# Optimization experiments

Hardware: AMD Instinct MI355X
Metric: run time of the kernel (lower is better)

The kernel has to match this reference:

```python
import jax, jax.numpy as jnp
import numpy as np

N_NODES = 100000
N_GRAPHS = 512
NEG_SLOPE = 0.2


def gat_layer(x, src, dst, W, a_src, a_dst, b):
    # PyG GATConv (heads=1, concat=True, add_self_loops handled by caller via src/dst)
    h = x @ W                                   # [N, F]
    e = jax.nn.leaky_relu((h @ a_src)[src] + (h @ a_dst)[dst], NEG_SLOPE)  # [E]
    m = jax.ops.segment_max(e, dst, num_segments=N_NODES)
    ex = jnp.exp(e - m[dst])
    s = jax.ops.segment_sum(ex, dst, num_segments=N_NODES)
    alpha = ex / (s[dst] + 1e-16)               # per-destination softmax
    out = jax.ops.segment_sum(alpha[:, None] * h[src], dst, num_segments=N_NODES)
    return out + b


def setup_inputs() -> dict:
    key = jax.random.key(0)
    ks = jax.random.split(key, 12)
    x = jax.random.normal(ks[0], (N_NODES, 5), dtype=jnp.float32)
    edge_index = jax.random.randint(ks[1], (2, 3200000), 0, N_NODES, dtype=jnp.int64)
    batch = jnp.sort(jax.random.randint(ks[2], (N_NODES,), 0, N_GRAPHS, dtype=jnp.int64))
    def glorot(k, shape):
        lim = float(np.sqrt(6.0 / (shape[0] + shape[-1])))
        return jax.random.uniform(k, shape, jnp.float32, -lim, lim)
    return {
        "x": x, "edge_index": edge_index, "batch": batch,
        "W1": glorot(ks[3], (5, 16)), "as1": glorot(ks[4], (16,)), "ad1": glorot(ks[5], (16,)), "b1": jnp.zeros((16,), jnp.float32),
        "W2": glorot(ks[6], (16, 16)), "as2": glorot(ks[7], (16,)), "ad2": glorot(ks[8], (16,)), "b2": jnp.zeros((16,), jnp.float32),
        "Wf": glorot(ks[9], (16, 2)), "bf": jnp.zeros((2,), jnp.float32),
    }


def reference(x, edge_index, batch, W1, as1, ad1, b1, W2, as2, ad2, b2, Wf, bf):
    # add self-loops (PyG GATConv default)
    loop = jnp.arange(N_NODES, dtype=edge_index.dtype)
    src = jnp.concatenate([edge_index[0], loop])
    dst = jnp.concatenate([edge_index[1], loop])
    h = jax.nn.relu(gat_layer(x, src, dst, W1, as1, ad1, b1))
    h = jax.nn.relu(gat_layer(h, src, dst, W2, as2, ad2, b2))
    # global mean pool over graphs
    sums = jax.ops.segment_sum(h, batch, num_segments=N_GRAPHS)
    cnt = jax.ops.segment_sum(jnp.ones((N_NODES,), h.dtype), batch, num_segments=N_GRAPHS)
    pooled = sums / jnp.maximum(cnt, 1.0)[:, None]   # [G, 16]
    return pooled @ Wf + bf                          # [G, 2]
```

## Files before the change

kernel.cpp:

```cpp
#include <hip/hip_runtime.h>
#include <hip/hip_fp16.h>
#include <math.h>

#define N_NODES 100000
#define N_GRAPHS 512
#define F 16
#define NEG_SLOPE 0.2f
#define DMAX 80
#define NSLOT 64
#define NBUCK 391
#define BCAP 8704
#define EPB 16

__device__ __forceinline__ float lrelu(float v) {
    return v > 0.0f ? v : NEG_SLOPE * v;
}

__device__ __forceinline__ unsigned fkey(float f) {
    unsigned b = __float_as_uint(f);
    return (b & 0x80000000u) ? ~b : (b | 0x80000000u);
}
__device__ __forceinline__ float funkey(unsigned k) {
    unsigned b = (k & 0x80000000u) ? (k ^ 0x80000000u) : ~k;
    return __uint_as_float(b);
}

__global__ void k_part_prep(const int* __restrict__ esrc,
                            const int* __restrict__ edst, int E0, int nT,
                            int* __restrict__ bcur,
                            unsigned* __restrict__ bucket,
                            const float* __restrict__ x,
                            const float* __restrict__ W1,
                            const float* __restrict__ as1,
                            const float* __restrict__ ad1,
                            __half* __restrict__ h1,
                            float* __restrict__ ssrc,
                            float* __restrict__ sdst,
                            unsigned* __restrict__ cs1,
                            unsigned* __restrict__ cd1) {
    __shared__ int hist[NBUCK];
    __shared__ int gbase[NBUCK];
    __shared__ int off[NBUCK];
    __shared__ unsigned ls[4], ld[4];

    if ((int)blockIdx.x < nT) {
        int tbase = blockIdx.x * (blockDim.x * EPB);
        for (int i = threadIdx.x; i < NBUCK; i += blockDim.x) hist[i] = 0;
        __syncthreads();

        int rb[EPB];
        unsigned rv[EPB];
#pragma unroll
        for (int i = 0; i < EPB; ++i) {
            int e = tbase + i * blockDim.x + threadIdx.x;
            rb[i] = -1;
            if (e < E0) {
                int d = edst[e];
                int s = esrc[e];
                int b = d >> 8;
                rb[i] = b;
                rv[i] = (unsigned)s | ((unsigned)(d & 255) << 17);
                atomicAdd(&hist[b], 1);
            }
        }
        __syncthreads();

        for (int b = threadIdx.x; b < NBUCK; b += blockDim.x) {
            int h = hist[b];
            gbase[b] = h ? atomicAdd(&bcur[b], h) : 0;
            off[b] = 0;
        }
        __syncthreads();

#pragma unroll
        for (int i = 0; i < EPB; ++i) {
            int b = rb[i];
            if (b >= 0) {
                int p = gbase[b] + atomicAdd(&off[b], 1);
                if (p < BCAP) bucket[(size_t)b * BCAP + p] = rv[i];
            }
        }
    } else {
        int n = (blockIdx.x - nT) * blockDim.x + threadIdx.x;
        float ss = -INFINITY, sd = -INFINITY;
        if (n < N_NODES) {
            float xi[5];
#pragma unroll
            for (int i = 0; i < 5; ++i) xi[i] = x[n * 5 + i];
            ss = 0.f; sd = 0.f;
#pragma unroll
            for (int f = 0; f < F; ++f) {
                float acc = 0.f;
#pragma unroll
                for (int i = 0; i < 5; ++i) acc += xi[i] * W1[i * F + f];
                h1[n * F + f] = __float2half(acc);
                ss += acc * as1[f];
                sd += acc * ad1[f];
            }
            ssrc[n] = ss;
            sdst[n] = sd;
        }
        unsigned ks = fkey(ss), kd = fkey(sd);
#pragma unroll
        for (int o = 32; o; o >>= 1) {
            ks = max(ks, (unsigned)__shfl_xor((int)ks, o, 64));
            kd = max(kd, (unsigned)__shfl_xor((int)kd, o, 64));
        }
        int wid = threadIdx.x >> 6, lane = threadIdx.x & 63;
        if (lane == 0) { ls[wid] = ks; ld[wid] = kd; }
        __syncthreads();
        if (threadIdx.x == 0) {
            unsigned ms = ls[0], md = ld[0];
#pragma unroll
            for (int w = 1; w < 4; ++w) { ms = max(ms, ls[w]); md = max(md, ld[w]); }
            atomicMax(&cs1[blockIdx.x & (NSLOT - 1)], ms);
            atomicMax(&cd1[blockIdx.x & (NSLOT - 1)], md);
        }
    }
}

__global__ void k_fill2(const int* __restrict__ bcur,
                        const unsigned* __restrict__ bucket,
                        int* __restrict__ col,
                        int* __restrict__ deg) {
    int b = blockIdx.x;
    __shared__ int cur[256];
    if (threadIdx.x < 256) cur[threadIdx.x] = 0;
    __syncthreads();
    int cnt = min(bcur[b], BCAP);
    const unsigned* bk = bucket + (size_t)b * BCAP;
    for (int i = threadIdx.x; i < cnt; i += blockDim.x) {
        unsigned v = __builtin_nontemporal_load(&bk[i]);
        int s = (int)(v & 0x1FFFFu);
        int dl = (int)(v >> 17);
        int r = atomicAdd(&cur[dl], 1);
        if (r < DMAX) col[((size_t)((b << 8) | dl)) * DMAX + r] = s;
    }
    __syncthreads();
    if (threadIdx.x < 256) {
        int dst = (b << 8) | threadIdx.x;
        if (dst < N_NODES) deg[dst] = min(cur[threadIdx.x], DMAX);
    }
}

__device__ __forceinline__ float gat_aggregate(int n, int lane,
                                               const int* __restrict__ deg,
                                               const int* __restrict__ col,
                                               const float* __restrict__ ssrc,
                                               const float* __restrict__ sdst,
                                               const __half* __restrict__ h,
                                               const float* __restrict__ b,
                                               float c) {
    int dg = deg[n];
    size_t st = (size_t)n * DMAX;
    float sd = sdst[n];
    float acc0 = 0.f, acc1 = 0.f, acc2 = 0.f, acc3 = 0.f, ssum = 0.f;
    int base = 0;
    for (; base + 32 <= dg; base += 32) {
        int srcA = __builtin_nontemporal_load(&col[st + base + lane]);
        int srcB = __builtin_nontemporal_load(&col[st + base + 16 + lane]);
        float peA = __expf(lrelu(ssrc[srcA] + sd) - c);
        float peB = __expf(lrelu(ssrc[srcB] + sd) - c);
        ssum += peA + peB;
#pragma unroll
        for (int k = 0; k < 16; k += 2) {
            int skA0 = __shfl(srcA, k, 16);
            float pkA0 = __shfl(peA, k, 16);
            int skA1 = __shfl(srcA, k + 1, 16);
            float pkA1 = __shfl(peA, k + 1, 16);
            acc0 += pkA0 * __half2float(h[skA0 * F + lane]);
            acc1 += pkA1 * __half2float(h[skA1 * F + lane]);
        }
#pragma unroll
        for (int k = 0; k < 16; k += 2) {
            int skB0 = __shfl(srcB, k, 16);
            float pkB0 = __shfl(peB, k, 16);
            int skB1 = __shfl(srcB, k + 1, 16);
            float pkB1 = __shfl(peB, k + 1, 16);
            acc2 += pkB0 * __half2float(h[skB0 * F + lane]);
            acc3 += pkB1 * __half2float(h[skB1 * F + lane]);
        }
    }
    for (; base + 16 <= dg; base += 16) {
        int src = __builtin_nontemporal_load(&col[st + base + lane]);
        float pe = __expf(lrelu(ssrc[src] + sd) - c);
        ssum += pe;
#pragma unroll
        for (int k = 0; k < 16; k += 2) {
            int sk0 = __shfl(src, k, 16);
            float pk0 = __shfl(pe, k, 16);
            int sk1 = __shfl(src, k + 1, 16);
            float pk1 = __shfl(pe, k + 1, 16);
            acc0 += pk0 * __half2float(h[sk0 * F + lane]);
            acc1 += pk1 * __half2float(h[sk1 * F + lane]);
        }
    }
    if (base < dg) {
        int j = base + lane;
        float pe = 0.f;
        int src = 0;
        if (j < dg) {
            src = __builtin_nontemporal_load(&col[st + j]);
            pe = __expf(lrelu(ssrc[src] + sd) - c);
        }
        ssum += pe;
        int cnt = dg - base;
        for (int k = 0; k < cnt; ++k) {
            int sk = __shfl(src, k, 16);
            float pk = __shfl(pe, k, 16);
            acc0 += pk * __half2float(h[sk * F + lane]);
        }
    }
    float acc = (acc0 + acc1) + (acc2 + acc3);
#pragma unroll
    for (int off = 8; off; off >>= 1) ssum += __shfl_xor(ssum, off, 16);
    float pes = __expf(lrelu(ssrc[n] + sd) - c);
    ssum += pes;
    acc += pes * __half2float(h[n * F + lane]);
    float of = acc / (ssum + 1e-16f) + b[lane];
    return of > 0.f ? of : 0.f;
}

__device__ __forceinline__ float slot_max_c(const unsigned* __restrict__ cs,
                                            const unsigned* __restrict__ cd) {
    unsigned ms = 0, md = 0;
#pragma unroll 8
    for (int i = 0; i < NSLOT; ++i) {
        ms = max(ms, cs[i]);
        md = max(md, cd[i]);
    }
    return lrelu(funkey(ms) + funkey(md));
}

__global__ void k_gather1(const int* __restrict__ deg,
                          const int* __restrict__ col,
                          const float* __restrict__ ssrc1,
                          const float* __restrict__ sdst1,
                          const __half* __restrict__ h1,
                          const float* __restrict__ b1,
                          const float* __restrict__ W2,
                          const float* __restrict__ as2,
                          const float* __restrict__ ad2,
                          __half* __restrict__ h2,
                          float* __restrict__ ssrc2,
                          float* __restrict__ sdst2,
                          const unsigned* __restrict__ cs1,
                          const unsigned* __restrict__ cd1,
                          unsigned* __restrict__ cs2,
                          unsigned* __restrict__ cd2) {
    int n = blockIdx.x * (blockDim.x >> 4) + (threadIdx.x >> 4);
    int lane = threadIdx.x & 15;
    float c1 = slot_max_c(cs1, cd1);
    float ho = gat_aggregate(n, lane, deg, col, ssrc1, sdst1, h1, b1, c1);

    float h2f = 0.f;
#pragma unroll
    for (int i = 0; i < F; ++i) {
        float hoi = __shfl(ho, i, 16);
        h2f += hoi * W2[i * F + lane];
    }
    h2[n * F + lane] = __float2half(h2f);

    float ps = h2f * as2[lane];
    float pd = h2f * ad2[lane];
#pragma unroll
    for (int off = 8; off; off >>= 1) {
        ps += __shfl_xor(ps, off, 16);
        pd += __shfl_xor(pd, off, 16);
    }
    if (lane == 0) { ssrc2[n] = ps; sdst2[n] = pd; }

    unsigned ks = fkey(ps), kd = fkey(pd);
#pragma unroll
    for (int off = 32; off; off >>= 1) {
        ks = max(ks, (unsigned)__shfl_xor((int)ks, off, 64));
        kd = max(kd, (unsigned)__shfl_xor((int)kd, off, 64));
    }
    __shared__ unsigned ls[4], ld[4];
    int wid = threadIdx.x >> 6, wl = threadIdx.x & 63;
    if (wl == 0) { ls[wid] = ks; ld[wid] = kd; }
    __syncthreads();
    if (threadIdx.x == 0) {
        unsigned ms = ls[0], md = ld[0];
#pragma unroll
        for (int w = 1; w < 4; ++w) { ms = max(ms, ls[w]); md = max(md, ld[w]); }
        atomicMax(&cs2[blockIdx.x & (NSLOT - 1)], ms);
        atomicMax(&cd2[blockIdx.x & (NSLOT - 1)], md);
    }
}

__global__ void k_gather2(const int* __restrict__ deg,
                          const int* __restrict__ col,
                          const float* __restrict__ ssrc2,
                          const float* __restrict__ sdst2,
                          const __half* __restrict__ h2,
                          const float* __restrict__ b2,
                          const int* __restrict__ batch,
                          float* __restrict__ gsum,
                          float* __restrict__ gcnt,
                          const unsigned* __restrict__ cs2,
                          const unsigned* __restrict__ cd2) {
    __shared__ float pool[4 * F];
    __shared__ float pcnt[4];
    if (threadIdx.x < 4 * F) pool[threadIdx.x] = 0.f;
    if (threadIdx.x < 4) pcnt[threadIdx.x] = 0.f;
    __syncthreads();

    int n = blockIdx.x * (blockDim.x >> 4) + (threadIdx.x >> 4);
    int lane = threadIdx.x & 15;
    float c2 = slot_max_c(cs2, cd2);
    float ho = gat_aggregate(n, lane, deg, col, ssrc2, sdst2, h2, b2, c2);

    int g = batch[n];
    int g0 = batch[blockIdx.x * (blockDim.x >> 4)];
    int idx = g - g0;
    if (idx < 4) {
        atomicAdd(&pool[idx * F + lane], ho);
        if (lane == 0) atomicAdd(&pcnt[idx], 1.f);
    } else {
        atomicAdd(&gsum[g * F + lane], ho);
        if (lane == 0) atomicAdd(&gcnt[g], 1.f);
    }
    __syncthreads();
    if (threadIdx.x < 4 * F) {
        float v = pool[threadIdx.x];
        if (v != 0.f)
            atomicAdd(&gsum[(g0 + (threadIdx.x >> 4)) * F + (threadIdx.x & 15)], v);
    }
    if (threadIdx.x < 4) {
        float cv = pcnt[threadIdx.x];
        if (cv != 0.f) atomicAdd(&gcnt[g0 + threadIdx.x], cv);
    }
}

__global__ void k_final(const float* __restrict__ gsum,
                        const float* __restrict__ gcnt,
                        const float* __restrict__ Wf,
                        const float* __restrict__ bf,
                        float* __restrict__ out) {
    int g = blockIdx.x * blockDim.x + threadIdx.x;
    if (g >= N_GRAPHS) return;
    float inv = 1.f / fmaxf(gcnt[g], 1.f);
    float o0 = bf[0], o1 = bf[1];
#pragma unroll
    for (int i = 0; i < F; ++i) {
        float p = gsum[g * F + i] * inv;
        o0 += p * Wf[i * 2 + 0];
        o1 += p * Wf[i * 2 + 1];
    }
    out[g * 2 + 0] = o0;
    out[g * 2 + 1] = o1;
}

extern "C" void kernel_launch(void* const* d_in, const int* in_sizes, int n_in,
                              void* d_out, int out_size, void* d_ws, size_t ws_size,
                              hipStream_t stream) {
    const float* x   = (const float*)d_in[0];
    const int*   ei  = (const int*)d_in[1];
    const int*   bat = (const int*)d_in[2];
    const float* W1  = (const float*)d_in[3];
    const float* as1 = (const float*)d_in[4];
    const float* ad1 = (const float*)d_in[5];
    const float* b1  = (const float*)d_in[6];
    const float* W2  = (const float*)d_in[7];
    const float* as2 = (const float*)d_in[8];
    const float* ad2 = (const float*)d_in[9];
    const float* b2  = (const float*)d_in[10];
    const float* Wf  = (const float*)d_in[11];
    const float* bf  = (const float*)d_in[12];
    float* out = (float*)d_out;

    const int E0 = in_sizes[1] / 2;
    const int* esrc = ei;
    const int* edst = ei + E0;

    __half* h1   = (__half*)d_ws;
    __half* h2   = h1 + (size_t)N_NODES * F;
    float* ssrc1 = (float*)(h2 + (size_t)N_NODES * F);
    float* sdst1 = ssrc1 + N_NODES;
    float* ssrc2 = sdst1 + N_NODES;
    float* sdst2 = ssrc2 + N_NODES;
    int*   col   = (int*)(sdst2 + N_NODES);
    int*   deg   = col + (size_t)N_NODES * DMAX;
    unsigned* bucket = (unsigned*)(deg + N_NODES);
    int*      zbase = (int*)(bucket + (size_t)NBUCK * BCAP);
    int*      bcur  = zbase;
    unsigned* cs1   = (unsigned*)(bcur + NBUCK);
    unsigned* cd1   = cs1 + NSLOT;
    unsigned* cs2   = cd1 + NSLOT;
    unsigned* cd2   = cs2 + NSLOT;
    float*    gsum  = (float*)(cd2 + NSLOT);
    float*    gcnt  = gsum + (size_t)N_GRAPHS * F;
    size_t zbytes = (size_t)(NBUCK + 4 * NSLOT + N_GRAPHS * F + N_GRAPHS) * 4;

    hipMemsetAsync(zbase, 0, zbytes, stream);

    const int BT = 256;
    const int nT = (E0 + BT * EPB - 1) / (BT * EPB);
    const int nN = (N_NODES + BT - 1) / BT;
    dim3 bPP(nT + nN);
    dim3 bB(NBUCK);
    dim3 bG16((N_NODES * 16) / BT);
    dim3 bG((N_GRAPHS + BT - 1) / BT);

    k_part_prep<<<bPP, BT, 0, stream>>>(esrc, edst, E0, nT, bcur, bucket,
                                        x, W1, as1, ad1, h1, ssrc1, sdst1, cs1, cd1);
    k_fill2<<<bB, 1024, 0, stream>>>(bcur, bucket, col, deg);
    k_gather1<<<bG16, BT, 0, stream>>>(deg, col, ssrc1, sdst1, h1, b1,
                                       W2, as2, ad2, h2, ssrc2, sdst2,
                                       cs1, cd1, cs2, cd2);
    k_gather2<<<bG16, BT, 0, stream>>>(deg, col, ssrc2, sdst2, h2, b2,
                                       bat, gsum, gcnt, cs2, cd2);
    k_final<<<bG, BT, 0, stream>>>(gsum, gcnt, Wf, bf, out);
}
```

Before: 279.3 us.

## Precompute packed edge weights in CSR and aggregate with 8 lanes per node

Layer-1 attention weights are now computed in the CSR fill kernel and packed as fp16 into the upper bits of each column entry beside the source index. A new k_pe2 pass rewrites those weights for layer 2. The gather kernels then use 8 lanes per node, each reading half2 feature pairs, and no longer do per-edge ssrc lookups or exp calls. The packing removes a dependent random load from the gather loop and halves lane count per node, at the cost of an extra kernel pass over col and fp16 precision for edge weights.

```diff
diff --git a/kernel.cpp b/kernel.cpp
--- a/kernel.cpp
+++ b/kernel.cpp
@@ -11,6 +11,7 @@
 #define NBUCK 391
 #define BCAP 8704
 #define EPB 16
+#define GPB 32
 
 __device__ __forceinline__ float lrelu(float v) {
     return v > 0.0f ? v : NEG_SLOPE * v;
@@ -23,6 +24,24 @@
 __device__ __forceinline__ float funkey(unsigned k) {
     unsigned b = (k & 0x80000000u) ? (k ^ 0x80000000u) : ~k;
     return __uint_as_float(b);
+}
+
+__device__ __forceinline__ float pe_unpack(unsigned v) {
+    return __half2float(__ushort_as_half((unsigned short)(v >> 17)));
+}
+__device__ __forceinline__ unsigned pe_pack(int s, float pe) {
+    return (unsigned)s | ((unsigned)__half_as_ushort(__float2half(pe)) << 17);
+}
+
+__device__ __forceinline__ float slot_max_c(const unsigned* __restrict__ cs,
+                                            const unsigned* __restrict__ cd) {
+    unsigned ms = 0, md = 0;
+#pragma unroll 8
+    for (int i = 0; i < NSLOT; ++i) {
+        ms = max(ms, cs[i]);
+        md = max(md, cd[i]);
+    }
+    return lrelu(funkey(ms) + funkey(md));
 }
 
 __global__ void k_part_prep(const int* __restrict__ esrc,
@@ -121,12 +140,22 @@
 
 __global__ void k_fill2(const int* __restrict__ bcur,
                         const unsigned* __restrict__ bucket,
-                        int* __restrict__ col,
+                        const float* __restrict__ ssrc1,
+                        const float* __restrict__ sdst1,
+                        const unsigned* __restrict__ cs1,
+                        const unsigned* __restrict__ cd1,
+                        unsigned* __restrict__ col,
                         int* __restrict__ deg) {
     int b = blockIdx.x;
     __shared__ int cur[256];
-    if (threadIdx.x < 256) cur[threadIdx.x] = 0;
+    __shared__ float sdl[256];
+    if (threadIdx.x < 256) {
+        cur[threadIdx.x] = 0;
+        int dst = (b << 8) | threadIdx.x;
+        sdl[threadIdx.x] = (dst < N_NODES) ? sdst1[dst] : 0.f;
+    }
     __syncthreads();
+    float c1 = slot_max_c(cs1, cd1);
     int cnt = min(bcur[b], BCAP);
     const unsigned* bk = bucket + (size_t)b * BCAP;
     for (int i = threadIdx.x; i < cnt; i += blockDim.x) {
@@ -134,7 +163,10 @@
         int s = (int)(v & 0x1FFFFu);
         int dl = (int)(v >> 17);
         int r = atomicAdd(&cur[dl], 1);
-        if (r < DMAX) col[((size_t)((b << 8) | dl)) * DMAX + r] = s;
+        if (r < DMAX) {
+            float pe = __expf(lrelu(ssrc1[s] + sdl[dl]) - c1);
+            col[((size_t)((b << 8) | dl)) * DMAX + r] = pe_pack(s, pe);
+        }
     }
     __syncthreads();
     if (threadIdx.x < 256) {
@@ -143,157 +175,152 @@
     }
 }
 
-__device__ __forceinline__ float gat_aggregate(int n, int lane,
-                                               const int* __restrict__ deg,
-                                               const int* __restrict__ col,
-                                               const float* __restrict__ ssrc,
-                                               const float* __restrict__ sdst,
-                                               const __half* __restrict__ h,
-                                               const float* __restrict__ b,
-                                               float c) {
+__device__ __forceinline__ float2 gat_agg8(int n, int l,
+                                           const int* __restrict__ deg,
+                                           const unsigned* __restrict__ col,
+                                           const float* __restrict__ ssrc,
+                                           const float* __restrict__ sdst,
+                                           const unsigned* __restrict__ hX,
+                                           const float* __restrict__ b,
+                                           float c) {
     int dg = deg[n];
     size_t st = (size_t)n * DMAX;
-    float sd = sdst[n];
-    float acc0 = 0.f, acc1 = 0.f, acc2 = 0.f, acc3 = 0.f, ssum = 0.f;
+    float ax = 0.f, ay = 0.f, ssum = 0.f;
     int base = 0;
-    for (; base + 32 <= dg; base += 32) {
-        int srcA = __builtin_nontemporal_load(&col[st + base + lane]);
-        int srcB = __builtin_nontemporal_load(&col[st + base + 16 + lane]);
-        float peA = __expf(lrelu(ssrc[srcA] + sd) - c);
-        float peB = __expf(lrelu(ssrc[srcB] + sd) - c);
-        ssum += peA + peB;
-#pragma unroll
-        for (int k = 0; k < 16; k += 2) {
-            int skA0 = __shfl(srcA, k, 16);
-            float pkA0 = __shfl(peA, k, 16);
-            int skA1 = __shfl(srcA, k + 1, 16);
-            float pkA1 = __shfl(peA, k + 1, 16);
-            acc0 += pkA0 * __half2float(h[skA0 * F + lane]);
-            acc1 += pkA1 * __half2float(h[skA1 * F + lane]);
-        }
-#pragma unroll
-        for (int k = 0; k < 16; k += 2) {
-            int skB0 = __shfl(srcB, k, 16);
-            float pkB0 = __shfl(peB, k, 16);
-            int skB1 = __shfl(srcB, k + 1, 16);
-            float pkB1 = __shfl(peB, k + 1, 16);
-            acc2 += pkB0 * __half2float(h[skB0 * F + lane]);
-            acc3 += pkB1 * __half2float(h[skB1 * F + lane]);
-        }
-    }
-    for (; base + 16 <= dg; base += 16) {
-        int src = __builtin_nontemporal_load(&col[st + base + lane]);
-        float pe = __expf(lrelu(ssrc[src] + sd) - c);
-        ssum += pe;
-#pragma unroll
-        for (int k = 0; k < 16; k += 2) {
-            int sk0 = __shfl(src, k, 16);
-            float pk0 = __shfl(pe, k, 16);
-            int sk1 = __shfl(src, k + 1, 16);
-            float pk1 = __shfl(pe, k + 1, 16);
-            acc0 += pk0 * __half2float(h[sk0 * F + lane]);
-            acc1 += pk1 * __half2float(h[sk1 * F + lane]);
+    for (; base + 8 <= dg; base += 8) {
+        unsigned v = __builtin_nontemporal_load(&col[st + base + l]);
+        ssum += pe_unpack(v);
+#pragma unroll
+        for (int k = 0; k < 8; ++k) {
+            unsigned vk = __shfl(v, k, 8);
+            int sk = (int)(vk & 0x1FFFFu);
+            float pk = pe_unpack(vk);
+            unsigned hw = hX[sk * 8 + l];
+            ax += pk * __half2float(__ushort_as_half((unsigned short)(hw & 0xFFFFu)));
+            ay += pk * __half2float(__ushort_as_half((unsigned short)(hw >> 16)));
         }
     }
     if (base < dg) {
-        int j = base + lane;
-        float pe = 0.f;
-        int src = 0;
+        int j = base + l;
+        unsigned v = 0;
         if (j < dg) {
-            src = __builtin_nontemporal_load(&col[st + j]);
-            pe = __expf(lrelu(ssrc[src] + sd) - c);
-        }
-        ssum += pe;
+            v = __builtin_nontemporal_load(&col[st + j]);
+            ssum += pe_unpack(v);
+        }
         int cnt = dg - base;
         for (int k = 0; k < cnt; ++k) {
-            int sk = __shfl(src, k, 16);
-            float pk = __shfl(pe, k, 16);
-            acc0 += pk * __half2float(h[sk * F + lane]);
-        }
-    }
-    float acc = (acc0 + acc1) + (acc2 + acc3);
-#pragma unroll
-    for (int off = 8; off; off >>= 1) ssum += __shfl_xor(ssum, off, 16);
-    float pes = __expf(lrelu(ssrc[n] + sd) - c);
+            unsigned vk = __shfl(v, k, 8);
+            int sk = (int)(vk & 0x1FFFFu);
+            float pk = pe_unpack(vk);
+            unsigned hw = hX[sk * 8 + l];
+            ax += pk * __half2float(__ushort_as_half((unsigned short)(hw & 0xFFFFu)));
+            ay += pk * __half2float(__ushort_as_half((unsigned short)(hw >> 16)));
+        }
+    }
+#pragma unroll
+    for (int o = 1; o < 8; o <<= 1) ssum += __shfl_xor(ssum, o, 8);
+    float pes = __expf(lrelu(ssrc[n] + sdst[n]) - c);
+    unsigned hw = hX[n * 8 + l];
+    ax += pes * __half2float(__ushort_as_half((unsigned short)(hw & 0xFFFFu)));
+    ay += pes * __half2float(__ushort_as_half((unsigned short)(hw >> 16)));
     ssum += pes;
-    acc += pes * __half2float(h[n * F + lane]);
-    float of = acc / (ssum + 1e-16f) + b[lane];
-    return of > 0.f ? of : 0.f;
-}
-
-__device__ __forceinline__ float slot_max_c(const unsigned* __restrict__ cs,
-                                            const unsigned* __restrict__ cd) {
-    unsigned ms = 0, md = 0;
-#pragma unroll 8
-    for (int i = 0; i < NSLOT; ++i) {
-        ms = max(ms, cs[i]);
-        md = max(md, cd[i]);
-    }
-    return lrelu(funkey(ms) + funkey(md));
+    float inv = 1.f / (ssum + 1e-16f);
+    float2 of;
+    of.x = fmaxf(ax * inv + b[2 * l], 0.f);
+    of.y = fmaxf(ay * inv + b[2 * l + 1], 0.f);
+    return of;
 }
 
 __global__ void k_gather1(const int* __restrict__ deg,
-                          const int* __restrict__ col,
+                          const unsigned* __restrict__ col,
                           const float* __restrict__ ssrc1,
                           const float* __restrict__ sdst1,
-                          const __half* __restrict__ h1,
+                          const unsigned* __restrict__ h1x,
                           const float* __restrict__ b1,
                           const float* __restrict__ W2,
                           const float* __restrict__ as2,
                           const float* __restrict__ ad2,
-                          __half* __restrict__ h2,
+                          unsigned* __restrict__ h2x,
                           float* __restrict__ ssrc2,
                           float* __restrict__ sdst2,
                           const unsigned* __restrict__ cs1,
                           const unsigned* __restrict__ cd1,
                           unsigned* __restrict__ cs2,
                           unsigned* __restrict__ cd2) {
-    int n = blockIdx.x * (blockDim.x >> 4) + (threadIdx.x >> 4);
-    int lane = threadIdx.x & 15;
+    __shared__ float lho[GPB][17];
+    __shared__ unsigned ls[4], ld[4];
+    int gid = threadIdx.x >> 3;
+    int l = threadIdx.x & 7;
+    int n = blockIdx.x * GPB + gid;
+
     float c1 = slot_max_c(cs1, cd1);
-    float ho = gat_aggregate(n, lane, deg, col, ssrc1, sdst1, h1, b1, c1);
-
-    float h2f = 0.f;
-#pragma unroll
-    for (int i = 0; i < F; ++i) {
-        float hoi = __shfl(ho, i, 16);
-        h2f += hoi * W2[i * F + lane];
-    }
-    h2[n * F + lane] = __float2half(h2f);
-
-    float ps = h2f * as2[lane];
-    float pd = h2f * ad2[lane];
-#pragma unroll
-    for (int off = 8; off; off >>= 1) {
-        ps += __shfl_xor(ps, off, 16);
-        pd += __shfl_xor(pd, off, 16);
-    }
-    if (lane == 0) { ssrc2[n] = ps; sdst2[n] = pd; }
+    float2 of = gat_agg8(n, l, deg, col, ssrc1, sdst1, h1x, b1, c1);
+
+    lho[gid][2 * l] = of.x;
+    lho[gid][2 * l + 1] = of.y;
+
+    float hx = 0.f, hy = 0.f;
+#pragma unroll
+    for (int i = 0; i < 16; ++i) {
+        float hoi = lho[gid][i];
+        hx += hoi * W2[i * F + 2 * l];
+        hy += hoi * W2[i * F + 2 * l + 1];
+    }
+    h2x[n * 8 + l] = (unsigned)__half_as_ushort(__float2half(hx)) |
+                     ((unsigned)__half_as_ushort(__float2half(hy)) << 16);
+
+    float ps = hx * as2[2 * l] + hy * as2[2 * l + 1];
+    float pd = hx * ad2[2 * l] + hy * ad2[2 * l + 1];
+#pragma unroll
+    for (int o = 1; o < 8; o <<= 1) {
+        ps += __shfl_xor(ps, o, 8);
+        pd += __shfl_xor(pd, o, 8);
+    }
+    if (l == 0) { ssrc2[n] = ps; sdst2[n] = pd; }
 
     unsigned ks = fkey(ps), kd = fkey(pd);
 #pragma unroll
-    for (int off = 32; off; off >>= 1) {
-        ks = max(ks, (unsigned)__shfl_xor((int)ks, off, 64));
-        kd = max(kd, (unsigned)__shfl_xor((int)kd, off, 64));
-    }
-    __shared__ unsigned ls[4], ld[4];
+    for (int o = 8; o < 64; o <<= 1) {
+        ks = max(ks, (unsigned)__shfl_xor((int)ks, o, 64));
+        kd = max(kd, (unsigned)__shfl_xor((int)kd, o, 64));
+    }
     int wid = threadIdx.x >> 6, wl = threadIdx.x & 63;
     if (wl == 0) { ls[wid] = ks; ld[wid] = kd; }
     __syncthreads();
     if (threadIdx.x == 0) {
-        unsigned ms = ls[0], md = ld[0];
-#pragma unroll
-        for (int w = 1; w < 4; ++w) { ms = max(ms, ls[w]); md = max(md, ld[w]); }
+        unsigned ms = max(max(ls[0], ls[1]), max(ls[2], ls[3]));
+        unsigned md = max(max(ld[0], ld[1]), max(ld[2], ld[3]));
         atomicMax(&cs2[blockIdx.x & (NSLOT - 1)], ms);
         atomicMax(&cd2[blockIdx.x & (NSLOT - 1)], md);
     }
 }
 
+__global__ void k_pe2(const int* __restrict__ deg,
+                      unsigned* __restrict__ col,
+                      const float* __restrict__ ssrc2,
+                      const float* __restrict__ sdst2,
+                      const unsigned* __restrict__ cs2,
+                      const unsigned* __restrict__ cd2) {
+    int gid = threadIdx.x >> 3;
+    int l = threadIdx.x & 7;
+    int n = blockIdx.x * GPB + gid;
+    float c2 = slot_max_c(cs2, cd2);
+    int dg = deg[n];
+    size_t st = (size_t)n * DMAX;
+    float sd = sdst2[n];
+    for (int j = l; j < dg; j += 8) {
+        unsigned v = col[st + j];
+        int s = (int)(v & 0x1FFFFu);
+        float pe = __expf(lrelu(ssrc2[s] + sd) - c2);
+        col[st + j] = pe_pack(s, pe);
+    }
+}
+
 __global__ void k_gather2(const int* __restrict__ deg,
-                          const int* __restrict__ col,
+                          const unsigned* __restrict__ col,
                           const float* __restrict__ ssrc2,
                           const float* __restrict__ sdst2,
-                          const __half* __restrict__ h2,
+                          const unsigned* __restrict__ h2x,
                           const float* __restrict__ b2,
                           const int* __restrict__ batch,
                           float* __restrict__ gsum,
@@ -306,20 +333,24 @@
     if (threadIdx.x < 4) pcnt[threadIdx.x] = 0.f;
     __syncthreads();
 
-    int n = blockIdx.x * (blockDim.x >> 4) + (threadIdx.x >> 4);
-    int lane = threadIdx.x & 15;
+    int gid = threadIdx.x >> 3;
+    int l = threadIdx.x & 7;
+    int n = blockIdx.x * GPB + gid;
+
     float c2 = slot_max_c(cs2, cd2);
-    float ho = gat_aggregate(n, lane, deg, col, ssrc2, sdst2, h2, b2, c2);
+    float2 of = gat_agg8(n, l, deg, col, ssrc2, sdst2, h2x, b2, c2);
 
     int g = batch[n];
-    int g0 = batch[blockIdx.x * (blockDim.x >> 4)];
+    int g0 = batch[blockIdx.x * GPB];
     int idx = g - g0;
     if (idx < 4) {
-        atomicAdd(&pool[idx * F + lane], ho);
-        if (lane == 0) atomicAdd(&pcnt[idx], 1.f);
+        atomicAdd(&pool[idx * F + 2 * l], of.x);
+        atomicAdd(&pool[idx * F + 2 * l + 1], of.y);
+        if (l == 0) atomicAdd(&pcnt[idx], 1.f);
     } else {
-        atomicAdd(&gsum[g * F + lane], ho);
-        if (lane == 0) atomicAdd(&gcnt[g], 1.f);
+        atomicAdd(&gsum[g * F + 2 * l], of.x);
+        atomicAdd(&gsum[g * F + 2 * l + 1], of.y);
+        if (l == 0) atomicAdd(&gcnt[g], 1.f);
     }
     __syncthreads();
     if (threadIdx.x < 4 * F) {
@@ -380,8 +411,8 @@
     float* sdst1 = ssrc1 + N_NODES;
     float* ssrc2 = sdst1 + N_NODES;
     float* sdst2 = ssrc2 + N_NODES;
-    int*   col   = (int*)(sdst2 + N_NODES);
-    int*   deg   = col + (size_t)N_NODES * DMAX;
+    unsigned* col = (unsigned*)(sdst2 + N_NODES);
+    int*   deg   = (int*)(col + (size_t)N_NODES * DMAX);
     unsigned* bucket = (unsigned*)(deg + N_NODES);
     int*      zbase = (int*)(bucket + (size_t)NBUCK * BCAP);
     int*      bcur  = zbase;
@@ -400,16 +431,17 @@
     const int nN = (N_NODES + BT - 1) / BT;
     dim3 bPP(nT + nN);
     dim3 bB(NBUCK);
-    dim3 bG16((N_NODES * 16) / BT);
+    dim3 bW(N_NODES / GPB);
     dim3 bG((N_GRAPHS + BT - 1) / BT);
 
     k_part_prep<<<bPP, BT, 0, stream>>>(esrc, edst, E0, nT, bcur, bucket,
                                         x, W1, as1, ad1, h1, ssrc1, sdst1, cs1, cd1);
-    k_fill2<<<bB, 1024, 0, stream>>>(bcur, bucket, col, deg);
-    k_gather1<<<bG16, BT, 0, stream>>>(deg, col, ssrc1, sdst1, h1, b1,
-                                       W2, as2, ad2, h2, ssrc2, sdst2,
-                                       cs1, cd1, cs2, cd2);
-    k_gather2<<<bG16, BT, 0, stream>>>(deg, col, ssrc2, sdst2, h2, b2,
-                                       bat, gsum, gcnt, cs2, cd2);
+    k_fill2<<<bB, 1024, 0, stream>>>(bcur, bucket, ssrc1, sdst1, cs1, cd1, col, deg);
+    k_gather1<<<bW, BT, 0, stream>>>(deg, col, ssrc1, sdst1, (const unsigned*)h1, b1,
+                                     W2, as2, ad2, (unsigned*)h2, ssrc2, sdst2,
+                                     cs1, cd1, cs2, cd2);
+    k_pe2<<<bW, BT, 0, stream>>>(deg, col, ssrc2, sdst2, cs2, cd2);
+    k_gather2<<<bW, BT, 0, stream>>>(deg, col, ssrc2, sdst2, (const unsigned*)h2, b2,
+                                     bat, gsum, gcnt, cs2, cd2);
     k_final<<<bG, BT, 0, stream>>>(gsum, gcnt, Wf, bf, out);
 }
```

Result: faster. 273.4 us (-2.1%).
